# Kernel tuning notes

Measured on AMD Instinct MI355X. Metric: run time of the kernel, lower is better.

Reference implementation:

```python
import jax, jax.numpy as jnp
import numpy as np

D_MODEL = 1024
NUM_HEADS = 16
HEAD_DIM = D_MODEL // NUM_HEADS


def setup_inputs() -> dict:
    key = jax.random.key(0)
    ks = jax.random.split(key, 5)
    x = jax.random.normal(ks[0], (2, 2048, D_MODEL), dtype=jnp.float32)
    s = 1.0 / np.sqrt(D_MODEL)
    # nn.Linear weight is [out, in]; y = x @ W.T
    Wq = jax.random.normal(ks[1], (D_MODEL, D_MODEL), dtype=jnp.float32) * s
    Wk = jax.random.normal(ks[2], (D_MODEL, D_MODEL), dtype=jnp.float32) * s
    Wv = jax.random.normal(ks[3], (D_MODEL, D_MODEL), dtype=jnp.float32) * s
    Wo = jax.random.normal(ks[4], (D_MODEL, D_MODEL), dtype=jnp.float32) * s
    return {"x": x, "Wq": Wq, "Wk": Wk, "Wv": Wv, "Wo": Wo}


def reference(x, Wq, Wk, Wv, Wo):
    b, s, d = x.shape
    h, hd = NUM_HEADS, HEAD_DIM
    # projections (Linear: x @ W.T), reshape to [b, h, s, hd]
    def proj(W):
        return (x @ W.T).reshape(b, s, h, hd).transpose(0, 2, 1, 3)
    Q, K, V = proj(Wq), proj(Wk), proj(Wv)
    # NOTE: original scales by 1/sqrt(d_model), not 1/sqrt(head_dim)
    scores = jnp.einsum('bhqd,bhkd->bhqk', Q, K) / jnp.sqrt(jnp.float32(d))
    attn = jax.nn.softmax(scores, axis=-1)
    ctx = jnp.einsum('bhqk,bhkd->bhqd', attn, V)
    ctx = ctx.transpose(0, 2, 1, 3).reshape(b, s, d)
    return ctx @ Wo.T
```

## Files before the change

kernel.cpp:

```cpp
#include <hip/hip_runtime.h>
#include <cstddef>
#include <cstdint>

#define SEQ 2048
#define DM 1024
#define NH 16
#define HD 64

typedef _Float16 f16;
typedef __attribute__((ext_vector_type(8))) _Float16 f16x8;
typedef __attribute__((ext_vector_type(4))) _Float16 f16x4;
typedef __attribute__((ext_vector_type(2))) _Float16 f16x2;
typedef __attribute__((ext_vector_type(4))) float f32x4;

__global__ __launch_bounds__(256) void cast_all(const float* __restrict__ x,
                                                const float* __restrict__ Wq,
                                                const float* __restrict__ Wk,
                                                const float* __restrict__ Wv,
                                                const float* __restrict__ Wo,
                                                f16* __restrict__ dst) {
  const int i = blockIdx.x * 256 + threadIdx.x;
  const float* src;
  int off;
  if (i < 1048576) {
    src = x; off = i;
  } else {
    const int j = i - 1048576;
    const int wsel = j >> 18;
    src = (wsel == 0) ? Wq : (wsel == 1) ? Wk : (wsel == 2) ? Wv : Wo;
    off = j & 262143;
  }
  const float4 v = ((const float4*)src)[off];
  f16x4 o = {(f16)v.x, (f16)v.y, (f16)v.z, (f16)v.w};
  ((f16x4*)dst)[i] = o;
}

__device__ __forceinline__ void gload16(const void* g, void* lds) {
  __builtin_amdgcn_global_load_lds((const __attribute__((address_space(1))) void*)g,
                                   (__attribute__((address_space(3))) void*)lds,
                                   16, 0, 0);
}

__device__ __forceinline__ void gemm_tile(const f16* __restrict__ A,
                                          const f16* __restrict__ B,
                                          f16* As, f16* Bs,
                                          int K, f32x4 acc[4][4]) {
  const int t = threadIdx.x;
  const int lane = t & 63;
  const int w = t >> 6;
  const int wm = (w & 1) << 6, wn = (w >> 1) << 6;
  const int srow = lane >> 3, sg = lane & 7;
  const int fr = lane & 15, q = lane >> 4;
  const int scol = (sg ^ srow) << 3;
  for (int k0 = 0; k0 < K; k0 += 64) {
    __syncthreads();
#pragma unroll
    for (int c = 0; c < 4; ++c) {
      const int row = (w << 5) + (c << 3) + srow;
      gload16(A + (size_t)row * K + k0 + scol, As + (w << 11) + (c << 9));
      gload16(B + (size_t)row * K + k0 + scol, Bs + (w << 11) + (c << 9));
    }
    __syncthreads();
    f16x8 af[4][2], bf[4][2];
#pragma unroll
    for (int i = 0; i < 4; ++i) {
      const int row = wm + (i << 4) + fr;
#pragma unroll
      for (int kh = 0; kh < 2; ++kh)
        af[i][kh] = *(const f16x8*)(As + row * 64 +
                                    ((((kh << 2) | q) ^ (row & 7)) << 3));
    }
#pragma unroll
    for (int j = 0; j < 4; ++j) {
      const int row = wn + (j << 4) + fr;
#pragma unroll
      for (int kh = 0; kh < 2; ++kh)
        bf[j][kh] = *(const f16x8*)(Bs + row * 64 +
                                    ((((kh << 2) | q) ^ (row & 7)) << 3));
    }
#pragma unroll
    for (int kh = 0; kh < 2; ++kh)
#pragma unroll
      for (int i = 0; i < 4; ++i)
#pragma unroll
        for (int j = 0; j < 4; ++j)
          acc[i][j] = __builtin_amdgcn_mfma_f32_16x16x32_f16(af[i][kh], bf[j][kh],
                                                             acc[i][j], 0, 0, 0);
  }
}

#define QSCALE 0.04508422003f
__global__ __launch_bounds__(256) void gemm_qkv(
    const f16* __restrict__ xb, const f16* __restrict__ Wqb,
    const f16* __restrict__ Wkb, const f16* __restrict__ Wvb,
    f16* __restrict__ Qb, f16* __restrict__ Kb, f16* __restrict__ Vtg) {
  __shared__ f16 smem[16384];
  f16* As = smem;
  f16* Bs = smem + 8192;
  const int which = blockIdx.x >> 3;
  const int bn = (blockIdx.x & 7) << 7;
  const int bm = blockIdx.y << 7;
  const f16* B = (which == 0) ? Wqb : (which == 1) ? Wkb : Wvb;
  f32x4 acc[4][4] = {};
  gemm_tile(xb + (size_t)bm * DM, B + (size_t)bn * DM, As, Bs, DM, acc);
  const int lane = threadIdx.x & 63, w = threadIdx.x >> 6;
  const int wm = (w & 1) << 6, wn = (w >> 1) << 6;
  const int col = lane & 15, q = lane >> 4;
  if (which < 2) {
    f16* C = (which == 0) ? Qb : Kb;
    const float sc = (which == 0) ? QSCALE : 1.0f;
#pragma unroll
    for (int i = 0; i < 4; ++i) {
      const int m = bm + wm + (i << 4) + (q << 2);
#pragma unroll
      for (int j = 0; j < 4; ++j) {
        const int n = bn + wn + (j << 4) + col;
#pragma unroll
        for (int r = 0; r < 4; ++r)
          C[(size_t)(m + r) * DM + n] = (f16)(acc[i][j][r] * sc);
      }
    }
  } else {
    __syncthreads();
#pragma unroll
    for (int i = 0; i < 4; ++i) {
      const int m0 = wm + (i << 4) + (q << 2);
      const int cm = m0 >> 3, sub = (m0 >> 2) & 1;
#pragma unroll
      for (int j = 0; j < 4; ++j) {
        const int nl = wn + (j << 4) + col;
        f16x4 o = {(f16)acc[i][j][0], (f16)acc[i][j][1],
                   (f16)acc[i][j][2], (f16)acc[i][j][3]};
        *(f16x4*)(smem + nl * 128 +
                  ((cm ^ (nl & 15) ^ ((nl >> 4) & 3)) << 3) + (sub << 2)) = o;
      }
    }
    __syncthreads();
    const int b = bm >> 11, sb = bm & 2047;
    const int d = threadIdx.x & 63;
#pragma unroll
    for (int step = 0; step < 16; ++step) {
      const int idx = (threadIdx.x >> 6) + (step << 2);
      const int hh = idx >> 5, s4 = idx & 31;
      const int nl = (hh << 6) + d;
      const int cm = s4 >> 1, sub = s4 & 1;
      const f16x4 v = *(const f16x4*)(smem + nl * 128 +
                                      ((cm ^ (nl & 15) ^ ((nl >> 4) & 3)) << 3) +
                                      (sub << 2));
      const int bh = (b << 4) + (bn >> 6) + hh;
      const int sg = sb + (s4 << 2);
      const size_t flat = ((size_t)bh << 17) + ((size_t)(sg >> 6) << 12) +
                          (((size_t)(s4 >> 2) & 3) << 10) +
                          (((size_t)s4 & 3) << 8) + ((size_t)d << 2);
      *(f16x4*)(Vtg + flat) = v;
    }
  }
}

__global__ __launch_bounds__(256) void gemm_out(const f16* __restrict__ Ab,
                                                const f16* __restrict__ Wob,
                                                float* __restrict__ out) {
  __shared__ f16 As[128 * 64];
  __shared__ f16 Bs[64 * 64];
  const int bn = blockIdx.x << 6, bm = blockIdx.y << 7;
  const int t = threadIdx.x, lane = t & 63, w = t >> 6;
  const int srow = lane >> 3, sg = lane & 7;
  const int fr = lane & 15, q = lane >> 4;
  const int scol = (sg ^ srow) << 3;
  const f16* A = Ab + (size_t)bm * DM;
  const f16* B = Wob + (size_t)bn * DM;
  const int wm = w << 5;
  f32x4 acc[2][4] = {};
  for (int k0 = 0; k0 < DM; k0 += 64) {
    __syncthreads();
#pragma unroll
    for (int c = 0; c < 4; ++c) {
      const int row = (w << 5) + (c << 3) + srow;
      gload16(A + (size_t)row * DM + k0 + scol, As + (w << 11) + (c << 9));
    }
#pragma unroll
    for (int c = 0; c < 2; ++c) {
      const int row = (w << 4) + (c << 3) + srow;
      gload16(B + (size_t)row * DM + k0 + scol, Bs + (w << 10) + (c << 9));
    }
    __syncthreads();
    f16x8 af[2][2], bf[4][2];
#pragma unroll
    for (int i = 0; i < 2; ++i) {
      const int row = wm + (i << 4) + fr;
#pragma unroll
      for (int kh = 0; kh < 2; ++kh)
        af[i][kh] = *(const f16x8*)(As + row * 64 +
                                    ((((kh << 2) | q) ^ (row & 7)) << 3));
    }
#pragma unroll
    for (int j = 0; j < 4; ++j) {
      const int row = (j << 4) + fr;
#pragma unroll
      for (int kh = 0; kh < 2; ++kh)
        bf[j][kh] = *(const f16x8*)(Bs + row * 64 +
                                    ((((kh << 2) | q) ^ (row & 7)) << 3));
    }
#pragma unroll
    for (int kh = 0; kh < 2; ++kh)
#pragma unroll
      for (int i = 0; i < 2; ++i)
#pragma unroll
        for (int j = 0; j < 4; ++j)
          acc[i][j] = __builtin_amdgcn_mfma_f32_16x16x32_f16(af[i][kh], bf[j][kh],
                                                             acc[i][j], 0, 0, 0);
  }
  const int col = lane & 15;
#pragma unroll
  for (int i = 0; i < 2; ++i) {
    const int m = bm + wm + (i << 4) + (q << 2);
#pragma unroll
    for (int j = 0; j < 4; ++j) {
      const int n = bn + (j << 4) + col;
#pragma unroll
      for (int r = 0; r < 4; ++r)
        out[(size_t)(m + r) * DM + n] = acc[i][j][r];
    }
  }
}

__global__ __launch_bounds__(256, 2) void attn_mfma(const f16* __restrict__ Qb,
                                                    const f16* __restrict__ Kb,
                                                    const f16* __restrict__ Vtg,
                                                    f16* __restrict__ Ctx) {
  __shared__ f16 smem[16384];
  const int t = threadIdx.x, lane = t & 63, w = t >> 6;
  const int fr = lane & 15, quad = lane >> 4;
  const int i = blockIdx.x;
  const int j = i >> 3;
  const int bh = ((i & 7) << 2) + (j >> 4);
  const int qt16 = j & 15;
  const int b = bh >> 4, h = bh & 15;

  const size_t qrow0 = (size_t)b * SEQ + qt16 * 128 + w * 32;

  f16x8 Qf[2][2];
#pragma unroll
  for (int qt = 0; qt < 2; ++qt)
#pragma unroll
    for (int hf = 0; hf < 2; ++hf)
      Qf[qt][hf] = *(const f16x8*)(Qb + (qrow0 + qt * 16 + fr) * DM + h * HD +
                                   hf * 32 + (quad << 3));

  const int krow = lane >> 2;
  const int kkc = ((lane & 3) - (lane >> 3)) & 3;
  const f16* Kg = Kb + ((size_t)b * SEQ + 16 * w + krow) * DM + h * HD + (kkc << 3);
  const f16* Vg = Vtg + ((size_t)bh << 17) + (((w << 7) + lane) << 3);

  const int crd = ((fr >> 1) << 3) | ((fr & 1) << 2) | (((fr >> 1) + quad) & 3);

  f16* K0 = smem;
  f16* K1 = smem + 4096;
  f16* V0 = smem + 8192;
  f16* V1 = smem + 12288;

  auto stage = [&](int kt, f16* Kimg, f16* Vimg) {
#pragma unroll
    for (int hf = 0; hf < 2; ++hf)
      gload16(Kg + (size_t)kt * 64 * DM + hf * 32,
              Kimg + (hf << 11) + (w << 9));
#pragma unroll
    for (int c = 0; c < 2; ++c)
      gload16(Vg + kt * 4096 + (c << 9), Vimg + (w << 10) + (c << 9));
  };

  f32x4 acc[2][4] = {};
  float lacc[2] = {0.f, 0.f};

  stage(0, K0, V0);

  auto body = [&](int kt, f16* KR, f16* VR, f16* KW, f16* VW) {
    __syncthreads();
    if (kt < 31) stage(kt + 1, KW, VW);

    f16x8 Kf[4][2];
#pragma unroll
    for (int mt = 0; mt < 4; ++mt)
#pragma unroll
      for (int hf = 0; hf < 2; ++hf)
        Kf[mt][hf] = *(const f16x8*)(KR + (crd << 3) + (hf << 11) + (mt << 9));
    f16x4 Vf[4][4];
#pragma unroll
    for (int dt = 0; dt < 4; ++dt)
#pragma unroll
      for (int kc = 0; kc < 4; ++kc)
        Vf[dt][kc] = *(const f16x4*)(VR + (kc << 10) + (quad << 8) +
                                     (((dt << 4) | fr) << 2));

    f32x4 z[2][4] = {};
#pragma unroll
    for (int hf = 0; hf < 2; ++hf)
#pragma unroll
      for (int qt = 0; qt < 2; ++qt)
#pragma unroll
        for (int mt = 0; mt < 4; ++mt)
          z[qt][mt] = __builtin_amdgcn_mfma_f32_16x16x32_f16(Kf[mt][hf], Qf[qt][hf],
                                                             z[qt][mt], 0, 0, 0);

    f16x4 pf[2][4];
#pragma unroll
    for (int qt = 0; qt < 2; ++qt)
#pragma unroll
      for (int mt = 0; mt < 4; ++mt) {
        const float p0 = __builtin_amdgcn_exp2f(z[qt][mt][0]);
        const float p1 = __builtin_amdgcn_exp2f(z[qt][mt][1]);
        const float p2 = __builtin_amdgcn_exp2f(z[qt][mt][2]);
        const float p3 = __builtin_amdgcn_exp2f(z[qt][mt][3]);
        lacc[qt] += (p0 + p1) + (p2 + p3);
        const f16x2 lo = __builtin_bit_cast(f16x2, __builtin_amdgcn_cvt_pkrtz(p0, p1));
        const f16x2 hi = __builtin_bit_cast(f16x2, __builtin_amdgcn_cvt_pkrtz(p2, p3));
        f16x4 pv; pv.x = lo.x; pv.y = lo.y; pv.z = hi.x; pv.w = hi.y;
        pf[qt][mt] = pv;
      }

#pragma unroll
    for (int kc = 0; kc < 4; ++kc)
#pragma unroll
      for (int dt = 0; dt < 4; ++dt)
#pragma unroll
        for (int qt = 0; qt < 2; ++qt)
          acc[qt][dt] = __builtin_amdgcn_mfma_f32_16x16x16f16(Vf[dt][kc], pf[qt][kc],
                                                              acc[qt][dt], 0, 0, 0);
  };

  for (int kt = 0; kt < 32; kt += 2) {
    body(kt, K0, V0, K1, V1);
    body(kt + 1, K1, V1, K0, V0);
  }

  float inv[2];
#pragma unroll
  for (int qt = 0; qt < 2; ++qt) {
    float l = lacc[qt];
    l += __shfl_xor(l, 16);
    l += __shfl_xor(l, 32);
    inv[qt] = __builtin_amdgcn_rcpf(l);
  }

  __syncthreads();
  f16* T = smem + (w << 11);
#pragma unroll
  for (int qt = 0; qt < 2; ++qt)
#pragma unroll
    for (int dt = 0; dt < 4; ++dt) {
      f16x4 o = {(f16)(acc[qt][dt][0] * inv[qt]), (f16)(acc[qt][dt][1] * inv[qt]),
                 (f16)(acc[qt][dt][2] * inv[qt]), (f16)(acc[qt][dt][3] * inv[qt])};
      *(f16x4*)(T + (qt * 16 + fr) * 64 + dt * 16 + (quad << 2)) = o;
    }
#pragma unroll
  for (int p = 0; p < 4; ++p) {
    const int ql = p * 8 + (lane >> 3);
    const f16x8 v = *(const f16x8*)(T + ql * 64 + ((lane & 7) << 3));
    *(f16x8*)(Ctx + (qrow0 + ql) * DM + h * HD + ((lane & 7) << 3)) = v;
  }
}

extern "C" void kernel_launch(void* const* d_in, const int* in_sizes, int n_in,
                              void* d_out, int out_size, void* d_ws, size_t ws_size,
                              hipStream_t stream) {
  const float* x  = (const float*)d_in[0];
  const float* Wq = (const float*)d_in[1];
  const float* Wk = (const float*)d_in[2];
  const float* Wv = (const float*)d_in[3];
  const float* Wo = (const float*)d_in[4];

  char* ws = (char*)d_ws;
  f16* xb  = (f16*)(ws);
  f16* Wb  = (f16*)(ws + (8u << 20));
  f16* Wqb = Wb;
  f16* Wkb = Wb + 1048576;
  f16* Wvb = Wb + 2097152;
  f16* Wob = Wb + 3145728;
  f16* Qb  = (f16*)(ws + (16u << 20));
  f16* Kb  = (f16*)(ws + (24u << 20));
  f16* Vtg = (f16*)(ws + (32u << 20));
  f16* Ctx = (f16*)(ws + (40u << 20));

  cast_all<<<8192, 256, 0, stream>>>(x, Wq, Wk, Wv, Wo, xb);

  gemm_qkv<<<dim3(24, 32), 256, 0, stream>>>(xb, Wqb, Wkb, Wvb, Qb, Kb, Vtg);
  attn_mfma<<<dim3(2 * NH * (SEQ / 128)), 256, 0, stream>>>(Qb, Kb, Vtg, Ctx);
  gemm_out<<<dim3(16, 32), 256, 0, stream>>>(Ctx, Wob, (float*)d_out);
}
```

Measured before the change: 182.1 us.

## Halve attention query tile per block to double grid and occupancy

The attention kernel now handles 64 query rows per block (16 per wave) instead of 128, doubling the grid to 1024 blocks and raising launch bounds to 4 blocks per CU. Per-wave accumulators and score registers are halved, which lowers register pressure and allows more waves in flight. In exchange, each K/V tile loaded into shared memory is reused by half as many queries, so global and LDS traffic for K/V per unit of work doubles.

```diff
diff --git a/kernel.cpp b/kernel.cpp
--- a/kernel.cpp
+++ b/kernel.cpp
@@ -224,7 +224,7 @@
   }
 }
 
-__global__ __launch_bounds__(256, 2) void attn_mfma(const f16* __restrict__ Qb,
+__global__ __launch_bounds__(256, 4) void attn_mfma(const f16* __restrict__ Qb,
                                                     const f16* __restrict__ Kb,
                                                     const f16* __restrict__ Vtg,
                                                     f16* __restrict__ Ctx) {
@@ -233,19 +233,17 @@
   const int fr = lane & 15, quad = lane >> 4;
   const int i = blockIdx.x;
   const int j = i >> 3;
-  const int bh = ((i & 7) << 2) + (j >> 4);
-  const int qt16 = j & 15;
+  const int bh = ((i & 7) << 2) + (j >> 5);
+  const int qt32 = j & 31;
   const int b = bh >> 4, h = bh & 15;
 
-  const size_t qrow0 = (size_t)b * SEQ + qt16 * 128 + w * 32;
-
-  f16x8 Qf[2][2];
-#pragma unroll
-  for (int qt = 0; qt < 2; ++qt)
-#pragma unroll
-    for (int hf = 0; hf < 2; ++hf)
-      Qf[qt][hf] = *(const f16x8*)(Qb + (qrow0 + qt * 16 + fr) * DM + h * HD +
-                                   hf * 32 + (quad << 3));
+  const size_t qrow0 = (size_t)b * SEQ + qt32 * 64 + w * 16;
+
+  f16x8 Qf[2];
+#pragma unroll
+  for (int hf = 0; hf < 2; ++hf)
+    Qf[hf] = *(const f16x8*)(Qb + (qrow0 + fr) * DM + h * HD +
+                             hf * 32 + (quad << 3));
 
   const int krow = lane >> 2;
   const int kkc = ((lane & 3) - (lane >> 3)) & 3;
@@ -269,8 +267,8 @@
       gload16(Vg + kt * 4096 + (c << 9), Vimg + (w << 10) + (c << 9));
   };
 
-  f32x4 acc[2][4] = {};
-  float lacc[2] = {0.f, 0.f};
+  f32x4 acc[4] = {};
+  float lacc = 0.f;
 
   stage(0, K0, V0);
 
@@ -292,40 +290,34 @@
         Vf[dt][kc] = *(const f16x4*)(VR + (kc << 10) + (quad << 8) +
                                      (((dt << 4) | fr) << 2));
 
-    f32x4 z[2][4] = {};
+    f32x4 z[4] = {};
 #pragma unroll
     for (int hf = 0; hf < 2; ++hf)
 #pragma unroll
-      for (int qt = 0; qt < 2; ++qt)
-#pragma unroll
-        for (int mt = 0; mt < 4; ++mt)
-          z[qt][mt] = __builtin_amdgcn_mfma_f32_16x16x32_f16(Kf[mt][hf], Qf[qt][hf],
-                                                             z[qt][mt], 0, 0, 0);
-
-    f16x4 pf[2][4];
-#pragma unroll
-    for (int qt = 0; qt < 2; ++qt)
-#pragma unroll
-      for (int mt = 0; mt < 4; ++mt) {
-        const float p0 = __builtin_amdgcn_exp2f(z[qt][mt][0]);
-        const float p1 = __builtin_amdgcn_exp2f(z[qt][mt][1]);
-        const float p2 = __builtin_amdgcn_exp2f(z[qt][mt][2]);
-        const float p3 = __builtin_amdgcn_exp2f(z[qt][mt][3]);
-        lacc[qt] += (p0 + p1) + (p2 + p3);
-        const f16x2 lo = __builtin_bit_cast(f16x2, __builtin_amdgcn_cvt_pkrtz(p0, p1));
-        const f16x2 hi = __builtin_bit_cast(f16x2, __builtin_amdgcn_cvt_pkrtz(p2, p3));
-        f16x4 pv; pv.x = lo.x; pv.y = lo.y; pv.z = hi.x; pv.w = hi.y;
-        pf[qt][mt] = pv;
-      }
+      for (int mt = 0; mt < 4; ++mt)
+        z[mt] = __builtin_amdgcn_mfma_f32_16x16x32_f16(Kf[mt][hf], Qf[hf],
+                                                       z[mt], 0, 0, 0);
+
+    f16x4 pf[4];
+#pragma unroll
+    for (int mt = 0; mt < 4; ++mt) {
+      const float p0 = __builtin_amdgcn_exp2f(z[mt][0]);
+      const float p1 = __builtin_amdgcn_exp2f(z[mt][1]);
+      const float p2 = __builtin_amdgcn_exp2f(z[mt][2]);
+      const float p3 = __builtin_amdgcn_exp2f(z[mt][3]);
+      lacc += (p0 + p1) + (p2 + p3);
+      const f16x2 lo = __builtin_bit_cast(f16x2, __builtin_amdgcn_cvt_pkrtz(p0, p1));
+      const f16x2 hi = __builtin_bit_cast(f16x2, __builtin_amdgcn_cvt_pkrtz(p2, p3));
+      f16x4 pv; pv.x = lo.x; pv.y = lo.y; pv.z = hi.x; pv.w = hi.y;
+      pf[mt] = pv;
+    }
 
 #pragma unroll
     for (int kc = 0; kc < 4; ++kc)
 #pragma unroll
       for (int dt = 0; dt < 4; ++dt)
-#pragma unroll
-        for (int qt = 0; qt < 2; ++qt)
-          acc[qt][dt] = __builtin_amdgcn_mfma_f32_16x16x16f16(Vf[dt][kc], pf[qt][kc],
-                                                              acc[qt][dt], 0, 0, 0);
+        acc[dt] = __builtin_amdgcn_mfma_f32_16x16x16f16(Vf[dt][kc], pf[kc],
+                                                        acc[dt], 0, 0, 0);
   };
 
   for (int kt = 0; kt < 32; kt += 2) {
@@ -333,28 +325,22 @@
     body(kt + 1, K1, V1, K0, V0);
   }
 
-  float inv[2];
-#pragma unroll
-  for (int qt = 0; qt < 2; ++qt) {
-    float l = lacc[qt];
-    l += __shfl_xor(l, 16);
-    l += __shfl_xor(l, 32);
-    inv[qt] = __builtin_amdgcn_rcpf(l);
-  }
+  float l = lacc;
+  l += __shfl_xor(l, 16);
+  l += __shfl_xor(l, 32);
+  const float inv = __builtin_amdgcn_rcpf(l);
 
   __syncthreads();
-  f16* T = smem + (w << 11);
-#pragma unroll
-  for (int qt = 0; qt < 2; ++qt)
-#pragma unroll
-    for (int dt = 0; dt < 4; ++dt) {
-      f16x4 o = {(f16)(acc[qt][dt][0] * inv[qt]), (f16)(acc[qt][dt][1] * inv[qt]),
-                 (f16)(acc[qt][dt][2] * inv[qt]), (f16)(acc[qt][dt][3] * inv[qt])};
-      *(f16x4*)(T + (qt * 16 + fr) * 64 + dt * 16 + (quad << 2)) = o;
-    }
-#pragma unroll
-  for (int p = 0; p < 4; ++p) {
-    const int ql = p * 8 + (lane >> 3);
+  f16* T = smem + (w << 10);
+#pragma unroll
+  for (int dt = 0; dt < 4; ++dt) {
+    f16x4 o = {(f16)(acc[dt][0] * inv), (f16)(acc[dt][1] * inv),
+               (f16)(acc[dt][2] * inv), (f16)(acc[dt][3] * inv)};
+    *(f16x4*)(T + fr * 64 + dt * 16 + (quad << 2)) = o;
+  }
+#pragma unroll
+  for (int p = 0; p < 2; ++p) {
+    const int ql = (p << 3) + (lane >> 3);
     const f16x8 v = *(const f16x8*)(T + ql * 64 + ((lane & 7) << 3));
     *(f16x8*)(Ctx + (qrow0 + ql) * DM + h * HD + ((lane & 7) << 3)) = v;
   }
@@ -384,6 +370,6 @@
   cast_all<<<8192, 256, 0, stream>>>(x, Wq, Wk, Wv, Wo, xb);
 
   gemm_qkv<<<dim3(24, 32), 256, 0, stream>>>(xb, Wqb, Wkb, Wvb, Qb, Kb, Vtg);
-  attn_mfma<<<dim3(2 * NH * (SEQ / 128)), 256, 0, stream>>>(Qb, Kb, Vtg, Ctx);
+  attn_mfma<<<dim3(2 * NH * (SEQ / 64)), 256, 0, stream>>>(Qb, Kb, Vtg, Ctx);
   gemm_out<<<dim3(16, 32), 256, 0, stream>>>(Ctx, Wob, (float*)d_out);
 }
```

Result: no change. 184.4 us (+1.3%).

## Software-pipeline attention loop and switch PV to 16x16x32 MFMA with new V layout

Applied to the files above, without the earlier changes.

The V-transpose epilogue of the projection kernel now writes 8-wide f16 chunks in a layout where each lane's 8 consecutive keys are contiguous. This lets the attention kernel load V fragments as f16x8 and use the 16x16x32 MFMA for P·V in place of pairs of 16x16x16 ones. The attention loop is also restructured so the P·V of the previous tile overlaps the fragment loads and QK/exp of the next tile, with a prologue and epilogue added. The cost is more live registers (Kf, Vf and pf held across stages), which may lower occupancy.

```diff
diff --git a/kernel.cpp b/kernel.cpp
--- a/kernel.cpp
+++ b/kernel.cpp
@@ -139,20 +139,30 @@
     const int b = bm >> 11, sb = bm & 2047;
     const int d = threadIdx.x & 63;
 #pragma unroll
-    for (int step = 0; step < 16; ++step) {
-      const int idx = (threadIdx.x >> 6) + (step << 2);
-      const int hh = idx >> 5, s4 = idx & 31;
+    for (int pr = 0; pr < 8; ++pr) {
+      const int idx0 = (threadIdx.x >> 6) + (pr << 3);
+      const int hh = idx0 >> 5;
+      const int s40 = idx0 & 31;
+      const int s41 = s40 + 4;
       const int nl = (hh << 6) + d;
-      const int cm = s4 >> 1, sub = s4 & 1;
-      const f16x4 v = *(const f16x4*)(smem + nl * 128 +
-                                      ((cm ^ (nl & 15) ^ ((nl >> 4) & 3)) << 3) +
-                                      (sub << 2));
+      f16x4 va, vb;
+      {
+        const int cm = s40 >> 1, sub = s40 & 1;
+        va = *(const f16x4*)(smem + nl * 128 +
+                             ((cm ^ (nl & 15) ^ ((nl >> 4) & 3)) << 3) + (sub << 2));
+      }
+      {
+        const int cm = s41 >> 1, sub = s41 & 1;
+        vb = *(const f16x4*)(smem + nl * 128 +
+                             ((cm ^ (nl & 15) ^ ((nl >> 4) & 3)) << 3) + (sub << 2));
+      }
       const int bh = (b << 4) + (bn >> 6) + hh;
-      const int sg = sb + (s4 << 2);
-      const size_t flat = ((size_t)bh << 17) + ((size_t)(sg >> 6) << 12) +
-                          (((size_t)(s4 >> 2) & 3) << 10) +
-                          (((size_t)s4 & 3) << 8) + ((size_t)d << 2);
-      *(f16x4*)(Vtg + flat) = v;
+      const int kt = (sb >> 6) + (s40 >> 4);
+      const int kc2 = (s40 & 15) >> 3, qd = s40 & 3;
+      const f16x8 vv = __builtin_shufflevector(va, vb, 0, 1, 2, 3, 4, 5, 6, 7);
+      const size_t flat = ((size_t)bh << 17) + ((size_t)kt << 12) +
+                          ((size_t)kc2 << 11) + ((size_t)qd << 9) + ((size_t)d << 3);
+      *(f16x8*)(Vtg + flat) = vv;
     }
   }
 }
@@ -262,8 +272,7 @@
   auto stage = [&](int kt, f16* Kimg, f16* Vimg) {
 #pragma unroll
     for (int hf = 0; hf < 2; ++hf)
-      gload16(Kg + (size_t)kt * 64 * DM + hf * 32,
-              Kimg + (hf << 11) + (w << 9));
+      gload16(Kg + (size_t)kt * 64 * DM + hf * 32, Kimg + (hf << 11) + (w << 9));
 #pragma unroll
     for (int c = 0; c < 2; ++c)
       gload16(Vg + kt * 4096 + (c << 9), Vimg + (w << 10) + (c << 9));
@@ -271,27 +280,23 @@
 
   f32x4 acc[2][4] = {};
   float lacc[2] = {0.f, 0.f};
-
-  stage(0, K0, V0);
-
-  auto body = [&](int kt, f16* KR, f16* VR, f16* KW, f16* VW) {
-    __syncthreads();
-    if (kt < 31) stage(kt + 1, KW, VW);
-
-    f16x8 Kf[4][2];
+  f16x8 Kf[4][2], Vf[4][2], pf[2][2];
+
+  auto frags = [&](const f16* KR, const f16* VR) {
 #pragma unroll
     for (int mt = 0; mt < 4; ++mt)
 #pragma unroll
       for (int hf = 0; hf < 2; ++hf)
         Kf[mt][hf] = *(const f16x8*)(KR + (crd << 3) + (hf << 11) + (mt << 9));
-    f16x4 Vf[4][4];
 #pragma unroll
     for (int dt = 0; dt < 4; ++dt)
 #pragma unroll
-      for (int kc = 0; kc < 4; ++kc)
-        Vf[dt][kc] = *(const f16x4*)(VR + (kc << 10) + (quad << 8) +
-                                     (((dt << 4) | fr) << 2));
-
+      for (int kc = 0; kc < 2; ++kc)
+        Vf[dt][kc] = *(const f16x8*)(VR + (kc << 11) + (quad << 9) +
+                                     (((dt << 4) | fr) << 3));
+  };
+
+  auto qkexp = [&]() {
     f32x4 z[2][4] = {};
 #pragma unroll
     for (int hf = 0; hf < 2; ++hf)
@@ -301,10 +306,9 @@
         for (int mt = 0; mt < 4; ++mt)
           z[qt][mt] = __builtin_amdgcn_mfma_f32_16x16x32_f16(Kf[mt][hf], Qf[qt][hf],
                                                              z[qt][mt], 0, 0, 0);
-
-    f16x4 pf[2][4];
-#pragma unroll
-    for (int qt = 0; qt < 2; ++qt)
+#pragma unroll
+    for (int qt = 0; qt < 2; ++qt) {
+      f16x4 p4[4];
 #pragma unroll
       for (int mt = 0; mt < 4; ++mt) {
         const float p0 = __builtin_amdgcn_exp2f(z[qt][mt][0]);
@@ -314,24 +318,50 @@
         lacc[qt] += (p0 + p1) + (p2 + p3);
         const f16x2 lo = __builtin_bit_cast(f16x2, __builtin_amdgcn_cvt_pkrtz(p0, p1));
         const f16x2 hi = __builtin_bit_cast(f16x2, __builtin_amdgcn_cvt_pkrtz(p2, p3));
-        f16x4 pv; pv.x = lo.x; pv.y = lo.y; pv.z = hi.x; pv.w = hi.y;
-        pf[qt][mt] = pv;
+        f16x4 pv4; pv4.x = lo.x; pv4.y = lo.y; pv4.z = hi.x; pv4.w = hi.y;
+        p4[mt] = pv4;
       }
-
-#pragma unroll
-    for (int kc = 0; kc < 4; ++kc)
+      pf[qt][0] = __builtin_shufflevector(p4[0], p4[1], 0, 1, 2, 3, 4, 5, 6, 7);
+      pf[qt][1] = __builtin_shufflevector(p4[2], p4[3], 0, 1, 2, 3, 4, 5, 6, 7);
+    }
+  };
+
+  auto pv = [&]() {
+#pragma unroll
+    for (int kc = 0; kc < 2; ++kc)
 #pragma unroll
       for (int dt = 0; dt < 4; ++dt)
 #pragma unroll
         for (int qt = 0; qt < 2; ++qt)
-          acc[qt][dt] = __builtin_amdgcn_mfma_f32_16x16x16f16(Vf[dt][kc], pf[qt][kc],
-                                                              acc[qt][dt], 0, 0, 0);
+          acc[qt][dt] = __builtin_amdgcn_mfma_f32_16x16x32_f16(Vf[dt][kc], pf[qt][kc],
+                                                               acc[qt][dt], 0, 0, 0);
   };
 
-  for (int kt = 0; kt < 32; kt += 2) {
-    body(kt, K0, V0, K1, V1);
-    body(kt + 1, K1, V1, K0, V0);
-  }
+  stage(0, K0, V0);
+
+  __syncthreads();
+  stage(1, K1, V1);
+  frags(K0, V0);
+  qkexp();
+
+  for (int kt = 1; kt < 31; kt += 2) {
+    __syncthreads();
+    stage(kt + 1, K0, V0);
+    pv();
+    frags(K1, V1);
+    qkexp();
+    __syncthreads();
+    stage(kt + 2, K1, V1);
+    pv();
+    frags(K0, V0);
+    qkexp();
+  }
+
+  __syncthreads();
+  pv();
+  frags(K1, V1);
+  qkexp();
+  pv();
 
   float inv[2];
 #pragma unroll
```

Measured after the change: 183.6 us. No clear change (+0.9%).
